# Optimization experiments

Measured on AMD Instinct MI355X. Metric: run time of the kernel, lower is better.

## Reference

```python
import jax, jax.numpy as jnp
import numpy as np

N_NODES = 50000
N_EDGES = 300000
D = 256  # node/edge feature dim; MLP input = 3*D = 768


def setup_inputs() -> dict:
    key = jax.random.key(0)
    ks = jax.random.split(key, 5)
    x_node = jax.random.normal(ks[0], (N_NODES, D), dtype=jnp.float32)
    x_edge = jax.random.normal(ks[1], (N_EDGES, D), dtype=jnp.float32)
    edge_index = jax.random.randint(ks[2], (2, N_EDGES), 0, N_NODES, dtype=jnp.int64)
    # MLP params: Linear(3*D, D) -> ReLU -> Linear(D, D)
    W1 = jax.random.normal(ks[3], (3 * D, D), dtype=jnp.float32) * (1.0 / np.sqrt(3 * D))
    b1 = jnp.zeros((D,), dtype=jnp.float32)
    W2 = jax.random.normal(ks[4], (D, D), dtype=jnp.float32) * (1.0 / np.sqrt(D))
    b2 = jnp.zeros((D,), dtype=jnp.float32)
    return {"x_node": x_node, "x_edge": x_edge, "edge_index": edge_index,
            "W1": W1, "b1": b1, "W2": W2, "b2": b2}


def reference(x_node, x_edge, edge_index, W1, b1, W2, b2):
    # gather src/dst node feats and concat with edge feats: [E, 3*D]
    src = x_node[edge_index[0]]
    dst = x_node[edge_index[1]]
    h = jnp.concatenate([src, dst, x_edge], axis=1)
    # MLP (custom_func): Linear -> ReLU -> Linear
    h = jax.nn.relu(h @ W1 + b1)
    x_edge_ = h @ W2 + b2
    return x_edge_
```

## Files before the change

kernel.cpp:

```cpp
#include <hip/hip_runtime.h>


typedef __attribute__((ext_vector_type(8))) short short8;
typedef __attribute__((ext_vector_type(4))) float f32x4;
typedef __attribute__((address_space(1))) unsigned int* gp1_t;
typedef __attribute__((address_space(3))) unsigned int* lp3_t;

#define SMEM_SZ 131072
#define LDO 260

__device__ __forceinline__ unsigned short f2b(float f) {
  unsigned int u = __float_as_uint(f);
  return (unsigned short)((u + 0x7FFFu + ((u >> 16) & 1u)) >> 16);
}
__device__ __forceinline__ unsigned int f2b2(float lo, float hi) {
  return (unsigned int)f2b(lo) | ((unsigned int)f2b(hi) << 16);
}
__device__ __forceinline__ void gload16(const void* g, void* l) {
  __builtin_amdgcn_global_load_lds((gp1_t)g, (lp3_t)l, 16, 0, 0);
}

__global__ void prep_w_kernel(const float* __restrict__ w,
                              unsigned short* __restrict__ wp, int total) {
  int i = blockIdx.x * 256 + threadIdx.x;
  if (i >= total) return;
  int step = i >> 14;
  int rem = i & 16383;
  int n = rem >> 6;
  int s = (rem >> 3) & 7;
  int j = i & 7;
  int k = step * 64 + (((s ^ (n & 7)) << 3) | j);
  wp[i] = f2b(w[(size_t)k * 256 + n]);
}

__global__ void conv_bf16_kernel(const float* __restrict__ x,
                                 unsigned short* __restrict__ y, int n4) {
  int i = blockIdx.x * 256 + threadIdx.x;
  if (i >= n4) return;
  float4 v = ((const float4*)x)[i];
  ushort4 u;
  u.x = f2b(v.x); u.y = f2b(v.y); u.z = f2b(v.z); u.w = f2b(v.w);
  ((ushort4*)y)[i] = u;
}

__global__ __launch_bounds__(512) void edge_mlp_full(
    const float* __restrict__ xnode, const float* __restrict__ xedge,
    const int* __restrict__ eidx,
    const unsigned short* __restrict__ nodeb, int use_nodeb,
    const unsigned short* __restrict__ wt1p, const float* __restrict__ b1,
    const unsigned short* __restrict__ wt2p, const float* __restrict__ b2,
    float* __restrict__ out, int E) {
  __shared__ __align__(16) char smem[SMEM_SZ];

  const int t = threadIdx.x, w = t >> 6, l = t & 63;
  const int lr = l & 15, lk = l >> 4;
  const int wr = w >> 2, wc = w & 3;
  const int ebase = blockIdx.x * 256;

  int nsrcq[4], ndstq[4];
#pragma unroll
  for (int q = 0; q < 4; ++q) {
    int rq = 32 * w + 8 * q + (l >> 3);
    int eq = ebase + rq;
    if (eq >= E) eq = E - 1;
    nsrcq[q] = eidx[eq];
    ndstq[q] = eidx[E + eq];
  }
  const int swz16 = ((l & 7) ^ ((l >> 3) & 7)) << 4;
  const int r2 = t >> 1;
  int e2 = ebase + r2;
  if (e2 >= E) e2 = E - 1;
  const int ns2 = eidx[e2], nd2 = eidx[E + e2];

  f32x4 acc[8][4];
#pragma unroll
  for (int i = 0; i < 8; ++i)
#pragma unroll
    for (int j = 0; j < 4; ++j) acc[i][j] = (f32x4)0.0f;

  auto stageB = [&](int step, int buf) {
    const char* g = (const char*)wt1p + (size_t)step * 32768 + (t << 4);
    char* d = smem + 65536 + buf * 32768 + (w << 10) + (l << 4);
#pragma unroll
    for (int q = 0; q < 4; ++q) gload16(g + q * 8192, d + q * 8192);
  };
  auto stageA_node = [&](int s, int buf) {
    const int colb = (s & 3) * 128;
    char* d = smem + buf * 32768 + (w << 12) + (l << 4);
#pragma unroll
    for (int q = 0; q < 4; ++q) {
      const int nid = (s < 4) ? nsrcq[q] : ndstq[q];
      gload16((const char*)nodeb + (size_t)nid * 512 + colb + swz16,
              d + (q << 10));
    }
  };
  auto stageA_f32 = [&](const float* base, int rowid, int coloff, int buf) {
    const int rb = r2 & 7;
    float4 v[8];
#pragma unroll
    for (int jj = 0; jj < 4; ++jj) {
      const int j = (t & 1) * 4 + jj;
      const float* p = base + (size_t)rowid * 256 + coloff + j * 8;
      v[2 * jj] = ((const float4*)p)[0];
      v[2 * jj + 1] = ((const float4*)p)[1];
    }
#pragma unroll
    for (int jj = 0; jj < 4; ++jj) {
      const int j = (t & 1) * 4 + jj;
      uint4 u;
      u.x = f2b2(v[2 * jj].x, v[2 * jj].y);
      u.y = f2b2(v[2 * jj].z, v[2 * jj].w);
      u.z = f2b2(v[2 * jj + 1].x, v[2 * jj + 1].y);
      u.w = f2b2(v[2 * jj + 1].z, v[2 * jj + 1].w);
      *(uint4*)(smem + buf * 32768 + r2 * 128 + ((j ^ rb) << 4)) = u;
    }
  };
  auto stageA = [&](int s, int buf) {
    if (s < 8) {
      if (use_nodeb) stageA_node(s, buf);
      else stageA_f32(xnode, (s < 4) ? ns2 : nd2, (s & 3) * 64, buf);
    } else {
      stageA_f32(xedge, e2, (s - 8) * 64, buf);
    }
  };
  auto compute = [&](int k) {
    const char* A = smem + (k & 1) * 32768;
    const char* B = smem + 65536 + (k & 1) * 32768;
    __builtin_amdgcn_s_setprio(1);
#pragma unroll
    for (int ks = 0; ks < 2; ++ks) {
      short8 bf[4];
#pragma unroll
      for (int ni = 0; ni < 4; ++ni) {
        const int n = wc * 64 + ni * 16 + lr;
        bf[ni] = *(const short8*)(B + n * 128 + (((ks * 4 + lk) ^ (n & 7)) << 4));
      }
#pragma unroll
      for (int mi = 0; mi < 8; ++mi) {
        const int m = wr * 128 + mi * 16 + lr;
        short8 af = *(const short8*)(A + m * 128 + (((ks * 4 + lk) ^ (m & 7)) << 4));
#pragma unroll
        for (int ni = 0; ni < 4; ++ni)
          acc[mi][ni] = __builtin_amdgcn_mfma_f32_16x16x32_bf16(
              af, bf[ni], acc[mi][ni], 0, 0, 0);
      }
    }
    __builtin_amdgcn_s_setprio(0);
  };

  stageA(0, 0);
  stageB(0, 0);
  __syncthreads();
  for (int k = 0; k < 12; ++k) {
    if (k + 1 < 12) {
      stageB(k + 1, (k + 1) & 1);
      stageA(k + 1, (k + 1) & 1);
    }
    compute(k);
    __syncthreads();
  }

  char* Hs = smem;
#pragma unroll
  for (int ni = 0; ni < 4; ++ni) {
    const int col = wc * 64 + ni * 16 + lr;
    const float bias = b1[col];
    const int cole = col & ~1;
    const int chunk = cole >> 3;
    const int cb = (cole & 6) * 2;
#pragma unroll
    for (int mi = 0; mi < 8; ++mi) {
      float v[4], p[4];
#pragma unroll
      for (int r = 0; r < 4; ++r) {
        float x = acc[mi][ni][r] + bias;
        v[r] = x > 0.f ? x : 0.f;
        acc[mi][ni][r] = 0.f;
      }
#pragma unroll
      for (int r = 0; r < 4; ++r) p[r] = __shfl_xor(v[r], 1, 64);
      const int r0 = (lr & 1) ? 2 : 0;
#pragma unroll
      for (int rr = 0; rr < 2; ++rr) {
        const int r = r0 + rr;
        const int row = wr * 128 + mi * 16 + lk * 4 + r;
        const float lo = (lr & 1) ? p[r] : v[r];
        const float hi = (lr & 1) ? v[r] : p[r];
        *(unsigned int*)(Hs + row * 512 + ((chunk ^ (row & 7)) << 4) + cb) =
            f2b2(lo, hi);
      }
    }
  }
  __syncthreads();

  short8 bfA[4], bfB[4];
  auto loadB2 = [&](int pair, short8 (&bf)[4]) {
    const char* wb = (const char*)wt2p + (pair >> 1) * 32768;
    const int ksl = (pair & 1) * 4 + lk;
#pragma unroll
    for (int ni = 0; ni < 4; ++ni) {
      const int n = wc * 64 + ni * 16 + lr;
      bf[ni] = *(const short8*)(wb + n * 128 + ((ksl ^ (n & 7)) << 4));
    }
  };
  auto mfmaH = [&](int pair, short8 (&bf)[4]) {
    const int j = (pair >> 1) * 8 + (pair & 1) * 4 + lk;
    __builtin_amdgcn_s_setprio(1);
#pragma unroll
    for (int mi = 0; mi < 8; ++mi) {
      const int m = wr * 128 + mi * 16 + lr;
      short8 af = *(const short8*)(Hs + m * 512 + ((j ^ (m & 7)) << 4));
#pragma unroll
      for (int ni = 0; ni < 4; ++ni)
        acc[mi][ni] = __builtin_amdgcn_mfma_f32_16x16x32_bf16(
            af, bf[ni], acc[mi][ni], 0, 0, 0);
    }
    __builtin_amdgcn_s_setprio(0);
  };
  loadB2(0, bfA);
#pragma unroll
  for (int pair = 0; pair < 8; pair += 2) {
    if (pair + 1 < 8) loadB2(pair + 1, bfB);
    mfmaH(pair, bfA);
    if (pair + 2 < 8) loadB2(pair + 2, bfA);
    if (pair + 1 < 8) mfmaH(pair + 1, bfB);
  }

  float* outst = (float*)smem;
#pragma unroll
  for (int p = 0; p < 4; ++p) {
    __syncthreads();
    if (wr == (p >> 1)) {
#pragma unroll
      for (int ni = 0; ni < 4; ++ni) {
        const int col = wc * 64 + ni * 16 + lr;
        const float bias = b2[col];
#pragma unroll
        for (int mh = 0; mh < 4; ++mh) {
          const int mi = (p & 1) * 4 + mh;
#pragma unroll
          for (int r = 0; r < 4; ++r)
            outst[(mh * 16 + lk * 4 + r) * LDO + col] = acc[mi][ni][r] + bias;
        }
      }
    }
    __syncthreads();
#pragma unroll
    for (int it = 0; it < 8; ++it) {
      const int idx = it * 2048 + t * 4;
      const int lrow = idx >> 8;
      const int cc = idx & 255;
      const int grow = ebase + p * 64 + lrow;
      if (grow < E)
        *(float4*)(out + (size_t)grow * 256 + cc) =
            *(const float4*)(outst + lrow * LDO + cc);
    }
  }
}

extern "C" void kernel_launch(void* const* d_in, const int* in_sizes, int n_in,
                              void* d_out, int out_size, void* d_ws, size_t ws_size,
                              hipStream_t stream) {
  const float* xnode = (const float*)d_in[0];
  const float* xedge = (const float*)d_in[1];
  const int* eidx = (const int*)d_in[2];
  const float* W1 = (const float*)d_in[3];
  const float* b1 = (const float*)d_in[4];
  const float* W2 = (const float*)d_in[5];
  const float* b2 = (const float*)d_in[6];
  float* out = (float*)d_out;

  const int NN = in_sizes[0] / 256;
  const int E = in_sizes[1] / 256;

  char* ws = (char*)d_ws;
  unsigned short* wt1p = (unsigned short*)ws;
  unsigned short* wt2p = (unsigned short*)(ws + 12 * 32768);
  unsigned short* nodeb = (unsigned short*)(ws + 16 * 32768);
  const size_t need_tbl = (size_t)16 * 32768 + (size_t)NN * 512;
  const int use_nodeb = (ws_size >= need_tbl) ? 1 : 0;

  prep_w_kernel<<<(12 * 16384 + 255) / 256, 256, 0, stream>>>(W1, wt1p,
                                                              12 * 16384);
  prep_w_kernel<<<(4 * 16384 + 255) / 256, 256, 0, stream>>>(W2, wt2p,
                                                             4 * 16384);
  if (use_nodeb) {
    const int n4 = NN * 64;
    conv_bf16_kernel<<<(n4 + 255) / 256, 256, 0, stream>>>(xnode, nodeb, n4);
  }

  const int grid = (E + 255) / 256;
  edge_mlp_full<<<grid, 512, 0, stream>>>(xnode, xedge, eidx, nodeb, use_nodeb,
                                          wt1p, b1, wt2p, b2, out, E);
}
```

Measured before the change: 372.0 us.

## Precompute per-node W1 projections and gather them instead of node features

The first linear layer is split by input block. The src and dst node parts are computed once per node (x_node @ W1_src and x_node @ W1_dst) in a new node_p_kernel and stored as bf16 tables. The edge kernel then runs only the edge-feature GEMM (K=256 instead of 768) and adds the gathered per-node projections in the epilogue before ReLU. This cuts the first-layer FLOPs per edge substantially, since there are far fewer nodes than edges. The cost is an extra kernel, a bf16 rounding of the partial sums, and scattered gathers of 256-wide rows in the epilogue. A fallback kernel covers the case where the workspace is too small.

Measured after the change: 385.4 us. 3.6% more time.

```diff
diff --git a/kernel.cpp b/kernel.cpp
--- a/kernel.cpp
+++ b/kernel.cpp
@@ -6,7 +6,6 @@
 typedef __attribute__((address_space(1))) unsigned int* gp1_t;
 typedef __attribute__((address_space(3))) unsigned int* lp3_t;
 
-#define SMEM_SZ 131072
 #define LDO 260
 
 __device__ __forceinline__ unsigned short f2b(float f) {
@@ -15,6 +14,9 @@
 }
 __device__ __forceinline__ unsigned int f2b2(float lo, float hi) {
   return (unsigned int)f2b(lo) | ((unsigned int)f2b(hi) << 16);
+}
+__device__ __forceinline__ float b2f(unsigned int u) {
+  return __uint_as_float((u & 0xffffu) << 16);
 }
 __device__ __forceinline__ void gload16(const void* g, void* l) {
   __builtin_amdgcn_global_load_lds((gp1_t)g, (lp3_t)l, 16, 0, 0);
@@ -33,44 +35,21 @@
   wp[i] = f2b(w[(size_t)k * 256 + n]);
 }
 
-__global__ void conv_bf16_kernel(const float* __restrict__ x,
-                                 unsigned short* __restrict__ y, int n4) {
-  int i = blockIdx.x * 256 + threadIdx.x;
-  if (i >= n4) return;
-  float4 v = ((const float4*)x)[i];
-  ushort4 u;
-  u.x = f2b(v.x); u.y = f2b(v.y); u.z = f2b(v.z); u.w = f2b(v.w);
-  ((ushort4*)y)[i] = u;
-}
-
-__global__ __launch_bounds__(512) void edge_mlp_full(
-    const float* __restrict__ xnode, const float* __restrict__ xedge,
-    const int* __restrict__ eidx,
-    const unsigned short* __restrict__ nodeb, int use_nodeb,
-    const unsigned short* __restrict__ wt1p, const float* __restrict__ b1,
-    const unsigned short* __restrict__ wt2p, const float* __restrict__ b2,
-    float* __restrict__ out, int E) {
-  __shared__ __align__(16) char smem[SMEM_SZ];
+__global__ __launch_bounds__(512) void node_p_kernel(
+    const float* __restrict__ xnode, const unsigned short* __restrict__ wtab,
+    unsigned short* __restrict__ Pbase, int NN) {
+  __shared__ __align__(16) char smem[65536];
 
   const int t = threadIdx.x, w = t >> 6, l = t & 63;
   const int lr = l & 15, lk = l >> 4;
   const int wr = w >> 2, wc = w & 3;
-  const int ebase = blockIdx.x * 256;
-
-  int nsrcq[4], ndstq[4];
-#pragma unroll
-  for (int q = 0; q < 4; ++q) {
-    int rq = 32 * w + 8 * q + (l >> 3);
-    int eq = ebase + rq;
-    if (eq >= E) eq = E - 1;
-    nsrcq[q] = eidx[eq];
-    ndstq[q] = eidx[E + eq];
-  }
-  const int swz16 = ((l & 7) ^ ((l >> 3) & 7)) << 4;
+  const int nbase = blockIdx.x * 256;
+  const char* wt = (const char*)wtab + blockIdx.y * 131072;
+  unsigned short* P = Pbase + (size_t)blockIdx.y * NN * 256;
+
   const int r2 = t >> 1;
-  int e2 = ebase + r2;
-  if (e2 >= E) e2 = E - 1;
-  const int ns2 = eidx[e2], nd2 = eidx[E + e2];
+  int row2 = nbase + r2;
+  if (row2 >= NN) row2 = NN - 1;
 
   f32x4 acc[8][4];
 #pragma unroll
@@ -78,29 +57,13 @@
 #pragma unroll
     for (int j = 0; j < 4; ++j) acc[i][j] = (f32x4)0.0f;
 
-  auto stageB = [&](int step, int buf) {
-    const char* g = (const char*)wt1p + (size_t)step * 32768 + (t << 4);
-    char* d = smem + 65536 + buf * 32768 + (w << 10) + (l << 4);
-#pragma unroll
-    for (int q = 0; q < 4; ++q) gload16(g + q * 8192, d + q * 8192);
-  };
-  auto stageA_node = [&](int s, int buf) {
-    const int colb = (s & 3) * 128;
-    char* d = smem + buf * 32768 + (w << 12) + (l << 4);
-#pragma unroll
-    for (int q = 0; q < 4; ++q) {
-      const int nid = (s < 4) ? nsrcq[q] : ndstq[q];
-      gload16((const char*)nodeb + (size_t)nid * 512 + colb + swz16,
-              d + (q << 10));
-    }
-  };
-  auto stageA_f32 = [&](const float* base, int rowid, int coloff, int buf) {
+  auto stageA = [&](int s, int buf) {
     const int rb = r2 & 7;
     float4 v[8];
 #pragma unroll
     for (int jj = 0; jj < 4; ++jj) {
       const int j = (t & 1) * 4 + jj;
-      const float* p = base + (size_t)rowid * 256 + coloff + j * 8;
+      const float* p = xnode + (size_t)row2 * 256 + s * 64 + j * 8;
       v[2 * jj] = ((const float4*)p)[0];
       v[2 * jj + 1] = ((const float4*)p)[1];
     }
@@ -115,13 +78,312 @@
       *(uint4*)(smem + buf * 32768 + r2 * 128 + ((j ^ rb) << 4)) = u;
     }
   };
+
+  stageA(0, 0);
+  __syncthreads();
+  for (int k = 0; k < 4; ++k) {
+    if (k + 1 < 4) stageA(k + 1, (k + 1) & 1);
+    const char* A = smem + (k & 1) * 32768;
+    const char* wb = wt + k * 32768;
+    __builtin_amdgcn_s_setprio(1);
+#pragma unroll
+    for (int ks = 0; ks < 2; ++ks) {
+      short8 bf[4];
+#pragma unroll
+      for (int ni = 0; ni < 4; ++ni) {
+        const int n = wc * 64 + ni * 16 + lr;
+        bf[ni] = *(const short8*)(wb + n * 128 + (((ks * 4 + lk) ^ (n & 7)) << 4));
+      }
+#pragma unroll
+      for (int mi = 0; mi < 8; ++mi) {
+        const int m = wr * 128 + mi * 16 + lr;
+        short8 af = *(const short8*)(A + m * 128 + (((ks * 4 + lk) ^ (m & 7)) << 4));
+#pragma unroll
+        for (int ni = 0; ni < 4; ++ni)
+          acc[mi][ni] = __builtin_amdgcn_mfma_f32_16x16x32_bf16(
+              af, bf[ni], acc[mi][ni], 0, 0, 0);
+      }
+    }
+    __builtin_amdgcn_s_setprio(0);
+    __syncthreads();
+  }
+
+#pragma unroll
+  for (int mi = 0; mi < 8; ++mi)
+#pragma unroll
+    for (int r = 0; r < 4; ++r) {
+      const int node = nbase + wr * 128 + mi * 16 + lk * 4 + r;
+      if (node < NN) {
+        uint2 o;
+        o.x = f2b2(acc[mi][0][r], acc[mi][1][r]);
+        o.y = f2b2(acc[mi][2][r], acc[mi][3][r]);
+        *(uint2*)((char*)P + (size_t)node * 512 + lr * 32 + wc * 8) = o;
+      }
+    }
+}
+
+__global__ __launch_bounds__(512) void edge_mlp_p(
+    const float* __restrict__ xedge, const int* __restrict__ eidx,
+    const unsigned short* __restrict__ Ps, const unsigned short* __restrict__ Pd,
+    const unsigned short* __restrict__ wt1ep, const float* __restrict__ b1,
+    const unsigned short* __restrict__ wt2p, const float* __restrict__ b2,
+    float* __restrict__ out, int E) {
+  __shared__ __align__(16) char smem[133120];
+
+  const int t = threadIdx.x, w = t >> 6, l = t & 63;
+  const int lr = l & 15, lk = l >> 4;
+  const int wr = w >> 2, wc = w & 3;
+  const int ebase = blockIdx.x * 256;
+
+  int* sIdx = (int*)(smem + 131072);
+  int* dIdx = (int*)(smem + 131072 + 1024);
+  {
+    const int i = t & 255;
+    int e = ebase + i;
+    if (e >= E) e = E - 1;
+    if (t < 256) sIdx[i] = eidx[e];
+    else         dIdx[i] = eidx[(size_t)E + e];
+  }
+
+  const int r2 = t >> 1;
+  int e2 = ebase + r2;
+  if (e2 >= E) e2 = E - 1;
+
+  f32x4 acc[8][4];
+#pragma unroll
+  for (int i = 0; i < 8; ++i)
+#pragma unroll
+    for (int j = 0; j < 4; ++j) acc[i][j] = (f32x4)0.0f;
+
+  auto stageB = [&](int step, int buf) {
+    const char* g = (const char*)wt1ep + (size_t)step * 32768 + (t << 4);
+    char* d = smem + 65536 + buf * 32768 + (w << 10) + (l << 4);
+#pragma unroll
+    for (int q = 0; q < 4; ++q) gload16(g + q * 8192, d + q * 8192);
+  };
   auto stageA = [&](int s, int buf) {
-    if (s < 8) {
-      if (use_nodeb) stageA_node(s, buf);
-      else stageA_f32(xnode, (s < 4) ? ns2 : nd2, (s & 3) * 64, buf);
-    } else {
-      stageA_f32(xedge, e2, (s - 8) * 64, buf);
-    }
+    const int rb = r2 & 7;
+    float4 v[8];
+#pragma unroll
+    for (int jj = 0; jj < 4; ++jj) {
+      const int j = (t & 1) * 4 + jj;
+      const float* p = xedge + (size_t)e2 * 256 + s * 64 + j * 8;
+      v[2 * jj] = ((const float4*)p)[0];
+      v[2 * jj + 1] = ((const float4*)p)[1];
+    }
+#pragma unroll
+    for (int jj = 0; jj < 4; ++jj) {
+      const int j = (t & 1) * 4 + jj;
+      uint4 u;
+      u.x = f2b2(v[2 * jj].x, v[2 * jj].y);
+      u.y = f2b2(v[2 * jj].z, v[2 * jj].w);
+      u.z = f2b2(v[2 * jj + 1].x, v[2 * jj + 1].y);
+      u.w = f2b2(v[2 * jj + 1].z, v[2 * jj + 1].w);
+      *(uint4*)(smem + buf * 32768 + r2 * 128 + ((j ^ rb) << 4)) = u;
+    }
+  };
+  auto compute = [&](int k) {
+    const char* A = smem + (k & 1) * 32768;
+    const char* B = smem + 65536 + (k & 1) * 32768;
+    __builtin_amdgcn_s_setprio(1);
+#pragma unroll
+    for (int ks = 0; ks < 2; ++ks) {
+      short8 bf[4];
+#pragma unroll
+      for (int ni = 0; ni < 4; ++ni) {
+        const int n = wc * 64 + ni * 16 + lr;
+        bf[ni] = *(const short8*)(B + n * 128 + (((ks * 4 + lk) ^ (n & 7)) << 4));
+      }
+#pragma unroll
+      for (int mi = 0; mi < 8; ++mi) {
+        const int m = wr * 128 + mi * 16 + lr;
+        short8 af = *(const short8*)(A + m * 128 + (((ks * 4 + lk) ^ (m & 7)) << 4));
+#pragma unroll
+        for (int ni = 0; ni < 4; ++ni)
+          acc[mi][ni] = __builtin_amdgcn_mfma_f32_16x16x32_bf16(
+              af, bf[ni], acc[mi][ni], 0, 0, 0);
+      }
+    }
+    __builtin_amdgcn_s_setprio(0);
+  };
+
+  stageA(0, 0);
+  stageB(0, 0);
+  __syncthreads();
+  for (int k = 0; k < 4; ++k) {
+    if (k + 1 < 4) {
+      stageB(k + 1, (k + 1) & 1);
+      stageA(k + 1, (k + 1) & 1);
+    }
+    compute(k);
+    __syncthreads();
+  }
+
+  char* Hs = smem;
+  float bias4[4];
+#pragma unroll
+  for (int ni = 0; ni < 4; ++ni) bias4[ni] = b1[wc * 64 + ni * 16 + lr];
+#pragma unroll
+  for (int mi = 0; mi < 8; ++mi) {
+    uint2 pls[4], pld[4];
+#pragma unroll
+    for (int r = 0; r < 4; ++r) {
+      const int m = wr * 128 + mi * 16 + lk * 4 + r;
+      const int si = sIdx[m], di = dIdx[m];
+      pls[r] = *(const uint2*)((const char*)Ps + (size_t)si * 512 + lr * 32 + wc * 8);
+      pld[r] = *(const uint2*)((const char*)Pd + (size_t)di * 512 + lr * 32 + wc * 8);
+    }
+#pragma unroll
+    for (int ni = 0; ni < 4; ++ni) {
+      const int col = wc * 64 + ni * 16 + lr;
+      const int cole = col & ~1;
+      const int chunk = cole >> 3;
+      const int cb = (cole & 6) * 2;
+      float v[4], p[4];
+#pragma unroll
+      for (int r = 0; r < 4; ++r) {
+        const unsigned us = (ni < 2) ? (pls[r].x >> (16 * ni)) : (pls[r].y >> (16 * (ni - 2)));
+        const unsigned ud = (ni < 2) ? (pld[r].x >> (16 * ni)) : (pld[r].y >> (16 * (ni - 2)));
+        float x = acc[mi][ni][r] + bias4[ni] + b2f(us) + b2f(ud);
+        v[r] = x > 0.f ? x : 0.f;
+        acc[mi][ni][r] = 0.f;
+      }
+#pragma unroll
+      for (int r = 0; r < 4; ++r) p[r] = __shfl_xor(v[r], 1, 64);
+      const int r0 = (lr & 1) ? 2 : 0;
+#pragma unroll
+      for (int rr = 0; rr < 2; ++rr) {
+        const int r = r0 + rr;
+        const int row = wr * 128 + mi * 16 + lk * 4 + r;
+        const float lo = (lr & 1) ? p[r] : v[r];
+        const float hi = (lr & 1) ? v[r] : p[r];
+        *(unsigned int*)(Hs + row * 512 + ((chunk ^ (row & 7)) << 4) + cb) =
+            f2b2(lo, hi);
+      }
+    }
+  }
+  __syncthreads();
+
+  short8 bfA[4], bfB[4];
+  auto loadB2 = [&](int pair, short8 (&bf)[4]) {
+    const char* wb = (const char*)wt2p + (pair >> 1) * 32768;
+    const int ksl = (pair & 1) * 4 + lk;
+#pragma unroll
+    for (int ni = 0; ni < 4; ++ni) {
+      const int n = wc * 64 + ni * 16 + lr;
+      bf[ni] = *(const short8*)(wb + n * 128 + ((ksl ^ (n & 7)) << 4));
+    }
+  };
+  auto mfmaH = [&](int pair, short8 (&bf)[4]) {
+    const int j = (pair >> 1) * 8 + (pair & 1) * 4 + lk;
+    __builtin_amdgcn_s_setprio(1);
+#pragma unroll
+    for (int mi = 0; mi < 8; ++mi) {
+      const int m = wr * 128 + mi * 16 + lr;
+      short8 af = *(const short8*)(Hs + m * 512 + ((j ^ (m & 7)) << 4));
+#pragma unroll
+      for (int ni = 0; ni < 4; ++ni)
+        acc[mi][ni] = __builtin_amdgcn_mfma_f32_16x16x32_bf16(
+            af, bf[ni], acc[mi][ni], 0, 0, 0);
+    }
+    __builtin_amdgcn_s_setprio(0);
+  };
+  loadB2(0, bfA);
+#pragma unroll
+  for (int pair = 0; pair < 8; pair += 2) {
+    if (pair + 1 < 8) loadB2(pair + 1, bfB);
+    mfmaH(pair, bfA);
+    if (pair + 2 < 8) loadB2(pair + 2, bfA);
+    if (pair + 1 < 8) mfmaH(pair + 1, bfB);
+  }
+
+  float* outst = (float*)smem;
+#pragma unroll
+  for (int p = 0; p < 4; ++p) {
+    __syncthreads();
+    if (wr == (p >> 1)) {
+#pragma unroll
+      for (int ni = 0; ni < 4; ++ni) {
+        const int col = wc * 64 + ni * 16 + lr;
+        const float bias = b2[col];
+#pragma unroll
+        for (int mh = 0; mh < 4; ++mh) {
+          const int mi = (p & 1) * 4 + mh;
+#pragma unroll
+          for (int r = 0; r < 4; ++r)
+            outst[(mh * 16 + lk * 4 + r) * LDO + col] = acc[mi][ni][r] + bias;
+        }
+      }
+    }
+    __syncthreads();
+#pragma unroll
+    for (int it = 0; it < 8; ++it) {
+      const int idx = it * 2048 + t * 4;
+      const int lrow = idx >> 8;
+      const int cc = idx & 255;
+      const int grow = ebase + p * 64 + lrow;
+      if (grow < E)
+        *(float4*)(out + (size_t)grow * 256 + cc) =
+            *(const float4*)(outst + lrow * LDO + cc);
+    }
+  }
+}
+
+__global__ __launch_bounds__(512) void edge_mlp_fb(
+    const float* __restrict__ xnode, const float* __restrict__ xedge,
+    const int* __restrict__ eidx,
+    const unsigned short* __restrict__ wt1p, const float* __restrict__ b1,
+    const unsigned short* __restrict__ wt2p, const float* __restrict__ b2,
+    float* __restrict__ out, int E) {
+  __shared__ __align__(16) char smem[131072];
+
+  const int t = threadIdx.x, w = t >> 6, l = t & 63;
+  const int lr = l & 15, lk = l >> 4;
+  const int wr = w >> 2, wc = w & 3;
+  const int ebase = blockIdx.x * 256;
+
+  const int r2 = t >> 1;
+  int e2 = ebase + r2;
+  if (e2 >= E) e2 = E - 1;
+  const int ns2 = eidx[e2], nd2 = eidx[(size_t)E + e2];
+
+  f32x4 acc[8][4];
+#pragma unroll
+  for (int i = 0; i < 8; ++i)
+#pragma unroll
+    for (int j = 0; j < 4; ++j) acc[i][j] = (f32x4)0.0f;
+
+  auto stageB = [&](int step, int buf) {
+    const char* g = (const char*)wt1p + (size_t)step * 32768 + (t << 4);
+    char* d = smem + 65536 + buf * 32768 + (w << 10) + (l << 4);
+#pragma unroll
+    for (int q = 0; q < 4; ++q) gload16(g + q * 8192, d + q * 8192);
+  };
+  auto stageA_f32 = [&](const float* base, int rowid, int coloff, int buf) {
+    const int rb = r2 & 7;
+    float4 v[8];
+#pragma unroll
+    for (int jj = 0; jj < 4; ++jj) {
+      const int j = (t & 1) * 4 + jj;
+      const float* p = base + (size_t)rowid * 256 + coloff + j * 8;
+      v[2 * jj] = ((const float4*)p)[0];
+      v[2 * jj + 1] = ((const float4*)p)[1];
+    }
+#pragma unroll
+    for (int jj = 0; jj < 4; ++jj) {
+      const int j = (t & 1) * 4 + jj;
+      uint4 u;
+      u.x = f2b2(v[2 * jj].x, v[2 * jj].y);
+      u.y = f2b2(v[2 * jj].z, v[2 * jj].w);
+      u.z = f2b2(v[2 * jj + 1].x, v[2 * jj + 1].y);
+      u.w = f2b2(v[2 * jj + 1].z, v[2 * jj + 1].w);
+      *(uint4*)(smem + buf * 32768 + r2 * 128 + ((j ^ rb) << 4)) = u;
+    }
+  };
+  auto stageA = [&](int s, int buf) {
+    if (s < 4)       stageA_f32(xnode, ns2, s * 64, buf);
+    else if (s < 8)  stageA_f32(xnode, nd2, (s - 4) * 64, buf);
+    else             stageA_f32(xedge, e2, (s - 8) * 64, buf);
   };
   auto compute = [&](int k) {
     const char* A = smem + (k & 1) * 32768;
@@ -272,24 +534,35 @@
 
   const int NN = in_sizes[0] / 256;
   const int E = in_sizes[1] / 256;
+  const int grid = (E + 255) / 256;
 
   char* ws = (char*)d_ws;
-  unsigned short* wt1p = (unsigned short*)ws;
-  unsigned short* wt2p = (unsigned short*)(ws + 12 * 32768);
-  unsigned short* nodeb = (unsigned short*)(ws + 16 * 32768);
-  const size_t need_tbl = (size_t)16 * 32768 + (size_t)NN * 512;
-  const int use_nodeb = (ws_size >= need_tbl) ? 1 : 0;
-
-  prep_w_kernel<<<(12 * 16384 + 255) / 256, 256, 0, stream>>>(W1, wt1p,
-                                                              12 * 16384);
-  prep_w_kernel<<<(4 * 16384 + 255) / 256, 256, 0, stream>>>(W2, wt2p,
-                                                             4 * 16384);
-  if (use_nodeb) {
-    const int n4 = NN * 64;
-    conv_bf16_kernel<<<(n4 + 255) / 256, 256, 0, stream>>>(xnode, nodeb, n4);
-  }
-
-  const int grid = (E + 255) / 256;
-  edge_mlp_full<<<grid, 512, 0, stream>>>(xnode, xedge, eidx, nodeb, use_nodeb,
-                                          wt1p, b1, wt2p, b2, out, E);
-}
+  const size_t need_new = 4 * 131072 + (size_t)2 * NN * 512;
+
+  if (ws_size >= need_new) {
+    unsigned short* wt1sp = (unsigned short*)ws;
+    unsigned short* wt1dp = (unsigned short*)(ws + 131072);
+    unsigned short* wt1ep = (unsigned short*)(ws + 262144);
+    unsigned short* wt2p  = (unsigned short*)(ws + 393216);
+    unsigned short* Ps    = (unsigned short*)(ws + 524288);
+    unsigned short* Pd    = Ps + (size_t)NN * 256;
+
+    prep_w_kernel<<<256, 256, 0, stream>>>(W1, wt1sp, 65536);
+    prep_w_kernel<<<256, 256, 0, stream>>>(W1 + 65536, wt1dp, 65536);
+    prep_w_kernel<<<256, 256, 0, stream>>>(W1 + 131072, wt1ep, 65536);
+    prep_w_kernel<<<256, 256, 0, stream>>>(W2, wt2p, 65536);
+
+    node_p_kernel<<<dim3((NN + 255) / 256, 2), 512, 0, stream>>>(xnode, wt1sp,
+                                                                 Ps, NN);
+    edge_mlp_p<<<grid, 512, 0, stream>>>(xedge, eidx, Ps, Pd, wt1ep, b1,
+                                         wt2p, b2, out, E);
+  } else {
+    unsigned short* wt1p = (unsigned short*)ws;
+    unsigned short* wt2p = (unsigned short*)(ws + 12 * 32768);
+    prep_w_kernel<<<(12 * 16384 + 255) / 256, 256, 0, stream>>>(W1, wt1p,
+                                                                12 * 16384);
+    prep_w_kernel<<<256, 256, 0, stream>>>(W2, wt2p, 65536);
+    edge_mlp_fb<<<grid, 512, 0, stream>>>(xnode, xedge, eidx, wt1p, b1,
+                                          wt2p, b2, out, E);
+  }
+}
```
